# Optimization experiments

Measured on AMD Instinct MI355X. Metric: run time of the kernel, lower is better.

Reference implementation:

```python
import jax, jax.numpy as jnp
import numpy as np

N, E, IN, H, O = 50000, 800000, 256, 8, 32


def setup_inputs() -> dict:
    key = jax.random.key(0)
    ks = jax.random.split(key, 8)
    feat = jax.random.normal(ks[0], (N, IN), dtype=jnp.float32)
    src = jax.random.randint(ks[1], (E,), 0, N, dtype=jnp.int32)
    dst = jax.random.randint(ks[2], (E,), 0, N, dtype=jnp.int32)
    # Xavier-normal-ish parameter init
    W = jax.random.normal(ks[3], (IN, H * O), dtype=jnp.float32) * (2.0 / (IN + H * O)) ** 0.5
    attn_l = jax.random.normal(ks[4], (H, O), dtype=jnp.float32) * (2.0 / (1 + H * O)) ** 0.5
    attn_r = jax.random.normal(ks[5], (H, O), dtype=jnp.float32) * (2.0 / (1 + H * O)) ** 0.5
    bias = jnp.zeros((H * O,), dtype=jnp.float32)
    return {"feat": feat, "W": W, "attn_l": attn_l, "attn_r": attn_r, "bias": bias, "src": src, "dst": dst}


def reference(feat, W, attn_l, attn_r, bias, src, dst):
    # Linear projection: [N, IN] @ [IN, H*O] -> [N, H, O]
    ft = (feat @ W).reshape(-1, H, O)
    # Additive attention logits per node, per head
    el = jnp.einsum('nho,ho->nh', ft, attn_l)  # [N, H]
    er = jnp.einsum('nho,ho->nh', ft, attn_r)  # [N, H]
    # Edge-wise: e = leaky_relu(el[u] + er[v])
    e = jax.nn.leaky_relu(el[src] + er[dst], negative_slope=0.2)  # [E, H]
    # Segment softmax over incoming edges of each destination node
    emax = jax.ops.segment_max(e, dst, num_segments=N)            # [N, H]
    ee = jnp.exp(e - emax[dst])                                   # [E, H]
    denom = jax.ops.segment_sum(ee, dst, num_segments=N)          # [N, H]
    a = ee / denom[dst]                                           # [E, H]
    # Weighted scatter-sum aggregation: sum_u a_{uv} * ft_u
    msg = ft[src] * a[:, :, None]                                 # [E, H, O]
    rst = jax.ops.segment_sum(msg, dst, num_segments=N)           # [N, H, O]
    rst = rst + bias.reshape(1, H, O)
    return rst
```

## Files before the change

kernel.cpp:

```cpp
#include <hip/hip_runtime.h>

#define N_NODES 50000
#define N_EDGES 800000
#define NPAD    50176
#define SPILL_CAP 8192

typedef __bf16 bf16x8 __attribute__((ext_vector_type(8)));
typedef float  fx4    __attribute__((ext_vector_type(4)));
typedef unsigned short us4 __attribute__((ext_vector_type(4)));
typedef unsigned short us8 __attribute__((ext_vector_type(8)));

__device__ __forceinline__ float b2f(unsigned short u) {
    return __uint_as_float(((unsigned)u) << 16);
}
__device__ __forceinline__ unsigned short f2b(float f) {
    unsigned x = __float_as_uint(f);
    return (unsigned short)((x + 0x7FFFu + ((x >> 16) & 1u)) >> 16);
}

__global__ __launch_bounds__(256) void prep_w(
    const float* __restrict__ W,
    const float* __restrict__ attn_l, const float* __restrict__ attn_r,
    unsigned short* __restrict__ Wt,
    unsigned short* __restrict__ M2t_hi, unsigned short* __restrict__ M2t_lo,
    int* __restrict__ cursor, int* __restrict__ spill_n) {
    int b = blockIdx.x, k = threadIdx.x;
    if (b < 256) {
        Wt[b * 256 + k] = f2b(W[k * 256 + b]);
    } else if (b < 272) {
        int j = b - 256;
        const float* av = (j < 8) ? (attn_l + j * 32) : (attn_r + (j - 8) * 32);
        int c0 = (j & 7) * 32;
        float s = 0.f;
#pragma unroll
        for (int o = 0; o < 32; ++o) s += W[k * 256 + c0 + o] * av[o];
        unsigned short h = f2b(s);
        M2t_hi[j * 256 + k] = h;
        M2t_lo[j * 256 + k] = f2b(s - b2f(h));
    } else {
        cursor[(b - 272) * 256 + k] = 0;
        if (b == 272 && k == 0) *spill_n = 0;
    }
}

__global__ __launch_bounds__(256) void gemm_ft(
    const float* __restrict__ feat,
    const unsigned short* __restrict__ Wt,
    const unsigned short* __restrict__ M2t_hi,
    const unsigned short* __restrict__ M2t_lo,
    unsigned short* __restrict__ ft,
    float* __restrict__ el, float* __restrict__ er,
    const int* __restrict__ src, const int* __restrict__ dst,
    int* __restrict__ cursor, unsigned short* __restrict__ inedge,
    int* __restrict__ spill_n, int2* __restrict__ spill, int stride) {
    __shared__ unsigned short Alds[64 * 264];
    __shared__ unsigned short Bounce[4][16 * 64];
    const int tid  = threadIdx.x;
    const int lane = tid & 63;
    const int wid  = tid >> 6;
    const int quad = lane >> 4, l15 = lane & 15;
    const int mbase = blockIdx.x * 64;
    const int nbase = wid * 64;

    fx4 acc[4][4];
    fx4 acce[4];
#pragma unroll
    for (int i = 0; i < 4; ++i) {
        acce[i] = (fx4)0.0f;
#pragma unroll
        for (int j = 0; j < 4; ++j) acc[i][j] = (fx4)0.0f;
    }

    {
        const int srow = tid >> 2, squart = tid & 3;
        int grow = mbase + srow;
        grow = grow < N_NODES ? grow : N_NODES - 1;
        const float* sp = feat + (size_t)grow * 256;
        unsigned short* sd = &Alds[srow * 264];
#pragma unroll
        for (int ii = 0; ii < 4; ++ii) {
            int c8 = ii * 8 + squart * 2;
            float4 f0 = *reinterpret_cast<const float4*>(sp + c8 * 8);
            float4 f1 = *reinterpret_cast<const float4*>(sp + c8 * 8 + 4);
            float4 f2 = *reinterpret_cast<const float4*>(sp + c8 * 8 + 8);
            float4 f3 = *reinterpret_cast<const float4*>(sp + c8 * 8 + 12);
            us8 p0, p1;
            p0[0] = f2b(f0.x); p0[1] = f2b(f0.y); p0[2] = f2b(f0.z); p0[3] = f2b(f0.w);
            p0[4] = f2b(f1.x); p0[5] = f2b(f1.y); p0[6] = f2b(f1.z); p0[7] = f2b(f1.w);
            p1[0] = f2b(f2.x); p1[1] = f2b(f2.y); p1[2] = f2b(f2.z); p1[3] = f2b(f2.w);
            p1[4] = f2b(f3.x); p1[5] = f2b(f3.y); p1[6] = f2b(f3.z); p1[7] = f2b(f3.w);
            *reinterpret_cast<us8*>(sd + c8 * 8) = p0;
            *reinterpret_cast<us8*>(sd + c8 * 8 + 8) = p1;
        }
    }
    __syncthreads();

    for (int k0 = 0; k0 < 256; k0 += 32) {
        const int krow = k0 + quad * 8;
        bf16x8 a[4], b[4];
#pragma unroll
        for (int mt = 0; mt < 4; ++mt)
            a[mt] = *reinterpret_cast<const bf16x8*>(&Alds[(mt * 16 + l15) * 264 + krow]);
#pragma unroll
        for (int nt = 0; nt < 4; ++nt)
            b[nt] = *reinterpret_cast<const bf16x8*>(Wt + (nbase + nt * 16 + l15) * 256 + krow);
#pragma unroll
        for (int mt = 0; mt < 4; ++mt)
#pragma unroll
            for (int nt = 0; nt < 4; ++nt)
                acc[mt][nt] = __builtin_amdgcn_mfma_f32_16x16x32_bf16(
                    a[mt], b[nt], acc[mt][nt], 0, 0, 0);
        if (wid == 0) {
            bf16x8 bh = *reinterpret_cast<const bf16x8*>(M2t_hi + l15 * 256 + krow);
            bf16x8 bl = *reinterpret_cast<const bf16x8*>(M2t_lo + l15 * 256 + krow);
#pragma unroll
            for (int mt = 0; mt < 4; ++mt) {
                acce[mt] = __builtin_amdgcn_mfma_f32_16x16x32_bf16(a[mt], bh, acce[mt], 0, 0, 0);
                acce[mt] = __builtin_amdgcn_mfma_f32_16x16x32_bf16(a[mt], bl, acce[mt], 0, 0, 0);
            }
        }
    }

    unsigned short* bw = Bounce[wid];
#pragma unroll
    for (int mt = 0; mt < 4; ++mt) {
#pragma unroll
        for (int r = 0; r < 4; ++r) {
            int rl = quad * 4 + r;
#pragma unroll
            for (int nt = 0; nt < 4; ++nt)
                bw[rl * 64 + nt * 16 + l15] = f2b(acc[mt][nt][r]);
        }
#pragma unroll
        for (int it = 0; it < 2; ++it) {
            int rl = (lane >> 3) + it * 8;
            int c8 = lane & 7;
            us8 v = *reinterpret_cast<const us8*>(&bw[rl * 64 + c8 * 8]);
            int grow = mbase + mt * 16 + rl;
            if (grow < N_NODES)
                *reinterpret_cast<us8*>(ft + (size_t)grow * 256 + nbase + c8 * 8) = v;
        }
    }
    if (wid == 0) {
#pragma unroll
        for (int mt = 0; mt < 4; ++mt) {
#pragma unroll
            for (int r = 0; r < 4; ++r) {
                int row = mbase + mt * 16 + quad * 4 + r;
                if (row < N_NODES) {
                    float v = acce[mt][r];
                    if (l15 < 8) el[row * 8 + l15] = v;
                    else         er[row * 8 + (l15 - 8)] = v;
                }
            }
        }
    }

    int t = blockIdx.x * 256 + tid;
    if (t < N_EDGES / 4) {
        int4 s4 = reinterpret_cast<const int4*>(src)[t];
        int4 d4 = reinterpret_cast<const int4*>(dst)[t];
        int ss[4] = {s4.x, s4.y, s4.z, s4.w};
        int dd[4] = {d4.x, d4.y, d4.z, d4.w};
#pragma unroll
        for (int i = 0; i < 4; ++i) {
            int idx = atomicAdd(&cursor[dd[i]], 1);
            if (idx < stride) {
                inedge[(size_t)dd[i] * stride + idx] = (unsigned short)ss[i];
            } else {
                int sp = atomicAdd(spill_n, 1);
                if (sp < SPILL_CAP) spill[sp] = make_int2(ss[i], dd[i]);
            }
        }
    }
}

__global__ __launch_bounds__(256) void aggregate(
    const unsigned short* __restrict__ ft,
    const float* __restrict__ el, const float* __restrict__ er,
    const int* __restrict__ cursor,
    const unsigned short* __restrict__ inedge,
    const int* __restrict__ spill_n, const int2* __restrict__ spill,
    const float* __restrict__ bias,
    float* __restrict__ out, int stride) {
    int wid = threadIdx.x >> 6, lane = threadIdx.x & 63;
    int v = blockIdx.x * 4 + wid;
    int deg_t = cursor[v];
    int deg = deg_t < stride ? deg_t : stride;
    int half = lane >> 5, l = lane & 31;
    int h = l >> 2;
    float erv = er[v * 8 + h];
    const unsigned short* ip = inedge + (size_t)v * stride;
    const us8* ft8 = reinterpret_cast<const us8*>(ft);

    float a[8] = {0.f, 0.f, 0.f, 0.f, 0.f, 0.f, 0.f, 0.f};
    float s = 0.f;
    int j = 0;
    for (; j + 8 <= deg; j += 8) {
        int u[4];
#pragma unroll
        for (int t = 0; t < 4; ++t) u[t] = ip[j + 2 * t + half];
        us8 f[4];
#pragma unroll
        for (int t = 0; t < 4; ++t) f[t] = ft8[(size_t)u[t] * 32 + l];
#pragma unroll
        for (int t = 0; t < 4; ++t) {
            float x = el[u[t] * 8 + h] + erv;
            x = x > 0.f ? x : 0.2f * x;
            float w = __expf(x);
            s += w;
#pragma unroll
            for (int i = 0; i < 8; ++i) a[i] += w * b2f(f[t][i]);
        }
    }
    for (; j + 2 <= deg; j += 2) {
        int u = ip[j + half];
        us8 f = ft8[(size_t)u * 32 + l];
        float x = el[u * 8 + h] + erv;
        x = x > 0.f ? x : 0.2f * x;
        float w = __expf(x);
        s += w;
#pragma unroll
        for (int i = 0; i < 8; ++i) a[i] += w * b2f(f[i]);
    }
    if (j < deg && half == 0) {
        int u = ip[j];
        us8 f = ft8[(size_t)u * 32 + l];
        float x = el[u * 8 + h] + erv;
        x = x > 0.f ? x : 0.2f * x;
        float w = __expf(x);
        s += w;
#pragma unroll
        for (int i = 0; i < 8; ++i) a[i] += w * b2f(f[i]);
    }
    if (deg_t > stride) {
        int sn = *spill_n;
        if (sn > SPILL_CAP) sn = SPILL_CAP;
        for (int t = 0; t < sn; ++t) {
            int2 e = spill[t];
            if (e.y == v && half == 0) {
                int u = e.x;
                us8 f = ft8[(size_t)u * 32 + l];
                float x = el[u * 8 + h] + erv;
                x = x > 0.f ? x : 0.2f * x;
                float w = __expf(x);
                s += w;
#pragma unroll
                for (int i = 0; i < 8; ++i) a[i] += w * b2f(f[i]);
            }
        }
    }
#pragma unroll
    for (int i = 0; i < 8; ++i) a[i] += __shfl_xor(a[i], 32);
    s += __shfl_xor(s, 32);
    float inv = deg_t > 0 ? 1.0f / s : 0.f;

    int fi = l * 2 + half;
    float4 bb = reinterpret_cast<const float4*>(bias)[fi];
    int base = half * 4;
    float4 o;
    o.x = a[base + 0] * inv + bb.x;
    o.y = a[base + 1] * inv + bb.y;
    o.z = a[base + 2] * inv + bb.z;
    o.w = a[base + 3] * inv + bb.w;
    reinterpret_cast<float4*>(out)[(size_t)v * 64 + fi] = o;
}

extern "C" void kernel_launch(void* const* d_in, const int* in_sizes, int n_in,
                              void* d_out, int out_size, void* d_ws, size_t ws_size,
                              hipStream_t stream) {
    const float* feat   = (const float*)d_in[0];
    const float* W      = (const float*)d_in[1];
    const float* attn_l = (const float*)d_in[2];
    const float* attn_r = (const float*)d_in[3];
    const float* bias   = (const float*)d_in[4];
    const int* src = (const int*)d_in[5];
    const int* dst = (const int*)d_in[6];
    float* out = (float*)d_out;

    char* ws = (char*)d_ws;
    unsigned short* Wt     = (unsigned short*)(ws + 0);
    unsigned short* M2t_hi = (unsigned short*)(ws + 131072);
    unsigned short* M2t_lo = (unsigned short*)(ws + 139264);
    unsigned short* ft     = (unsigned short*)(ws + 147456);
    float* el              = (float*)(ws + 25747456);
    float* er              = (float*)(ws + 27347456);
    int* cursor            = (int*)(ws + 28947456);
    int* spill_n           = (int*)(ws + 29148160);
    int2* spill            = (int2*)(ws + 29148224);
    unsigned short* inedge = (unsigned short*)(ws + 29213760);

    size_t avail = ws_size > 29213760ull ? ws_size - 29213760ull : 0;
    int stride = (int)(avail / (2ull * NPAD));
    if (stride > 64) stride = 64;

    prep_w<<<468, 256, 0, stream>>>(W, attn_l, attn_r, Wt, M2t_hi, M2t_lo,
                                    cursor, spill_n);
    gemm_ft<<<782, 256, 0, stream>>>(feat, Wt, M2t_hi, M2t_lo, ft, el, er,
                                     src, dst, cursor, inedge, spill_n, spill,
                                     stride);
    aggregate<<<12500, 256, 0, stream>>>(ft, el, er, cursor, inedge,
                                         spill_n, spill, bias, out, stride);
}
```

Measured before the change: 245.8 us.

## Split edge bucketing into its own kernel and reuse GEMM LDS for bounce

Edge bucketing moves out of the GEMM kernel into a separate one-edge-per-thread kernel that runs before the GEMM. The GEMM now reuses its A-tile shared buffer, behind a barrier, as the epilogue bounce buffer, which cuts its LDS footprint. The aim is higher GEMM occupancy and no atomic-heavy tail on the GEMM blocks, at the cost of an extra kernel launch and scattered atomics that no longer overlap with GEMM work.

```diff
diff --git a/kernel.cpp b/kernel.cpp
--- a/kernel.cpp
+++ b/kernel.cpp
@@ -43,18 +43,31 @@
     }
 }
 
+__global__ __launch_bounds__(256) void bucket(
+    const int* __restrict__ src, const int* __restrict__ dst,
+    int* __restrict__ cursor, unsigned short* __restrict__ inedge,
+    int* __restrict__ spill_n, int2* __restrict__ spill, int stride) {
+    int t = blockIdx.x * 256 + threadIdx.x;
+    if (t < N_EDGES) {
+        int s = src[t], d = dst[t];
+        int idx = atomicAdd(&cursor[d], 1);
+        if (idx < stride) {
+            inedge[(size_t)d * stride + idx] = (unsigned short)s;
+        } else {
+            int sp = atomicAdd(spill_n, 1);
+            if (sp < SPILL_CAP) spill[sp] = make_int2(s, d);
+        }
+    }
+}
+
 __global__ __launch_bounds__(256) void gemm_ft(
     const float* __restrict__ feat,
     const unsigned short* __restrict__ Wt,
     const unsigned short* __restrict__ M2t_hi,
     const unsigned short* __restrict__ M2t_lo,
     unsigned short* __restrict__ ft,
-    float* __restrict__ el, float* __restrict__ er,
-    const int* __restrict__ src, const int* __restrict__ dst,
-    int* __restrict__ cursor, unsigned short* __restrict__ inedge,
-    int* __restrict__ spill_n, int2* __restrict__ spill, int stride) {
+    float* __restrict__ el, float* __restrict__ er) {
     __shared__ unsigned short Alds[64 * 264];
-    __shared__ unsigned short Bounce[4][16 * 64];
     const int tid  = threadIdx.x;
     const int lane = tid & 63;
     const int wid  = tid >> 6;
@@ -120,8 +133,9 @@
             }
         }
     }
-
-    unsigned short* bw = Bounce[wid];
+    __syncthreads();
+
+    unsigned short* bw = &Alds[wid * 1024];
 #pragma unroll
     for (int mt = 0; mt < 4; ++mt) {
 #pragma unroll
@@ -152,24 +166,6 @@
                     if (l15 < 8) el[row * 8 + l15] = v;
                     else         er[row * 8 + (l15 - 8)] = v;
                 }
-            }
-        }
-    }
-
-    int t = blockIdx.x * 256 + tid;
-    if (t < N_EDGES / 4) {
-        int4 s4 = reinterpret_cast<const int4*>(src)[t];
-        int4 d4 = reinterpret_cast<const int4*>(dst)[t];
-        int ss[4] = {s4.x, s4.y, s4.z, s4.w};
-        int dd[4] = {d4.x, d4.y, d4.z, d4.w};
-#pragma unroll
-        for (int i = 0; i < 4; ++i) {
-            int idx = atomicAdd(&cursor[dd[i]], 1);
-            if (idx < stride) {
-                inedge[(size_t)dd[i] * stride + idx] = (unsigned short)ss[i];
-            } else {
-                int sp = atomicAdd(spill_n, 1);
-                if (sp < SPILL_CAP) spill[sp] = make_int2(ss[i], dd[i]);
             }
         }
     }
@@ -296,9 +292,9 @@
 
     prep_w<<<468, 256, 0, stream>>>(W, attn_l, attn_r, Wt, M2t_hi, M2t_lo,
                                     cursor, spill_n);
-    gemm_ft<<<782, 256, 0, stream>>>(feat, Wt, M2t_hi, M2t_lo, ft, el, er,
-                                     src, dst, cursor, inedge, spill_n, spill,
-                                     stride);
+    bucket<<<3125, 256, 0, stream>>>(src, dst, cursor, inedge,
+                                     spill_n, spill, stride);
+    gemm_ft<<<782, 256, 0, stream>>>(feat, Wt, M2t_hi, M2t_lo, ft, el, er);
     aggregate<<<12500, 256, 0, stream>>>(ft, el, er, cursor, inedge,
                                          spill_n, spill, bias, out, stride);
 }
```

Measured after the change: 247.0 us. Within noise of the previous version (+0.5%).
